# Kernel optimization log

Hardware: AMD Instinct MI355X
Metric: run time of the kernel (lower is better)

Reference implementation:

```python
import jax, jax.numpy as jnp
import numpy as np

B, D, S, E = 32768, 512, 128, 8


def setup_inputs() -> dict:
    key = jax.random.key(0)
    ks = jax.random.split(key, 8)
    x = jax.random.normal(ks[0], (B, D), dtype=jnp.float32)
    y_index = jax.random.randint(ks[1], (B, 1), 0, E, dtype=jnp.int32)
    y_hard = jax.random.uniform(ks[2], (B, E), dtype=jnp.float32)
    z = jax.random.normal(ks[3], (B, 1), dtype=jnp.float32)
    # per-branch 2-layer MLP params, kaiming-ish scaling
    W1 = jax.random.normal(ks[4], (E, D, S), dtype=jnp.float32) / np.sqrt(D)
    b1 = jax.random.normal(ks[5], (E, S), dtype=jnp.float32) * 0.01
    W2 = jax.random.normal(ks[6], (E, S, D), dtype=jnp.float32) / np.sqrt(S)
    b2 = jax.random.normal(ks[7], (E, D), dtype=jnp.float32) * 0.01
    return {"x": x, "y_index": y_index, "y_hard": y_hard, "z": z,
            "W1": W1, "b1": b1, "W2": W2, "b2": b2}


def reference(x, y_index, y_hard, z, W1, b1, W2, b2):
    # out = relu(x); each token b routed to branch y_index[b];
    # branch MLP: relu(out @ W1[e] + b1[e]) @ W2[e] + b2[e], scaled by z, plus residual.
    # y_hard unused (eval path / backward_on_y_hard=False).
    n_branches = W1.shape[0]
    yi = y_index[:, 0]                                   # [B]
    onehot = jax.nn.one_hot(yi, n_branches, dtype=x.dtype)  # [B,E]
    out = jax.nn.relu(x)                                 # [B,D]
    h = jax.nn.relu(jnp.einsum('bd,eds->bes', out, W1) + b1[None])  # [B,E,S]
    h_sel = jnp.einsum('bes,be->bs', h, onehot)          # [B,S] hidden of routed branch
    o = jnp.einsum('bs,esd->bed', h_sel, W2)             # [B,E,D]
    o_sel = jnp.einsum('bed,be->bd', o, onehot) + b2[yi] # [B,D]
    return x + o_sel * z
```

## Files before the change

kernel.cpp:

```cpp
#include <hip/hip_runtime.h>
#include <hip/hip_bf16.h>

#define NB 32768
#define ND 512
#define NS 128
#define NE 8
#define TPE 96

typedef __attribute__((ext_vector_type(8))) short bf16x8;
typedef __attribute__((ext_vector_type(4))) float f32x4;

__device__ __forceinline__ unsigned short f2b(float f) {
  union { __hip_bfloat16 h; unsigned short u; } cv;
  cv.h = __float2bfloat16(f);
  return cv.u;
}

__device__ __forceinline__ bf16x8 relu_cvt8v(float4 a, float4 b) {
  bf16x8 r;
  r[0] = (short)f2b(fmaxf(a.x, 0.f)); r[1] = (short)f2b(fmaxf(a.y, 0.f));
  r[2] = (short)f2b(fmaxf(a.z, 0.f)); r[3] = (short)f2b(fmaxf(a.w, 0.f));
  r[4] = (short)f2b(fmaxf(b.x, 0.f)); r[5] = (short)f2b(fmaxf(b.y, 0.f));
  r[6] = (short)f2b(fmaxf(b.z, 0.f)); r[7] = (short)f2b(fmaxf(b.w, 0.f));
  return r;
}

__device__ __forceinline__ void gload16(const void* gsrc, void* ldst) {
  __builtin_amdgcn_global_load_lds(
      (const __attribute__((address_space(1))) unsigned int*)gsrc,
      (__attribute__((address_space(3))) unsigned int*)ldst, 16, 0, 0);
}

#define BARV6  asm volatile("s_waitcnt vmcnt(6)\n\ts_barrier" ::: "memory")
#define BARV12 asm volatile("s_waitcnt vmcnt(12)\n\ts_barrier" ::: "memory")
#define BARV10 asm volatile("s_waitcnt vmcnt(10)\n\ts_barrier" ::: "memory")
#define BARV0  asm volatile("s_waitcnt vmcnt(0)\n\ts_barrier" ::: "memory")
#define BARL   asm volatile("s_waitcnt lgkmcnt(0)\n\ts_barrier" ::: "memory")
#define BARV2L asm volatile("s_waitcnt vmcnt(2) lgkmcnt(0)\n\ts_barrier" ::: "memory")
#define CFENCE asm volatile("" ::: "memory")

__global__ void zero_counts_k(int* counts) {
  if (threadIdx.x < NE) counts[threadIdx.x] = 0;
}

__global__ void bin_rows_k(const int* __restrict__ yidx, int* __restrict__ counts,
                           int* __restrict__ bucket) {
  __shared__ int lcnt[NE];
  __shared__ int lbase[NE];
  int tid = threadIdx.x;
  if (tid < NE) lcnt[tid] = 0;
  __syncthreads();
  int b = blockIdx.x * blockDim.x + tid;
  int e = yidx[b];
  int pos = atomicAdd(&lcnt[e], 1);
  __syncthreads();
  if (tid < NE) lbase[tid] = atomicAdd(&counts[tid], lcnt[tid]);
  __syncthreads();
  bucket[e * NB + lbase[e] + pos] = b;
}

__global__ void transpose_cvt_k(const float* __restrict__ in,
                                unsigned short* __restrict__ out, int R, int C) {
  __shared__ float lt[32][33];
  int tpm = (R >> 5) * (C >> 5);
  int mat = blockIdx.x / tpm;
  int rem = blockIdx.x % tpm;
  int tcn = C >> 5;
  int tr = rem / tcn, tc = rem % tcn;
  const float* mi = in + (size_t)mat * R * C;
  unsigned short* mo = out + (size_t)mat * R * C;
  int r = threadIdx.x >> 5, c = threadIdx.x & 31;
#pragma unroll
  for (int i = 0; i < 4; ++i) {
    int rr = r + i * 8;
    lt[rr][c] = mi[(size_t)(tr * 32 + rr) * C + tc * 32 + c];
  }
  __syncthreads();
#pragma unroll
  for (int i = 0; i < 4; ++i) {
    int rr = r + i * 8;
    int orow = tc * 32 + rr;
    int d = tr * 32 + c;
    int ocol = (d & ~63) | ((d & 63) ^ ((orow & 7) << 3));
    mo[(size_t)orow * R + ocol] = f2b(lt[c][rr]);
  }
}

#define M1LOADX(DST, c)                                 \
  do {                                                  \
    const float* xp = xrow + (c) * 64;                  \
    DST[0] = *(const float4*)(xp);                      \
    DST[1] = *(const float4*)(xp + 4);                  \
    DST[2] = *(const float4*)(xp + 32);                 \
    DST[3] = *(const float4*)(xp + 36);                 \
  } while (0)

#define M1STAGE(c)                                                        \
  do {                                                                    \
    gload16(g0 + (c) * 128, (char*)wt[(c) % 3] + p0 * 16);                \
    gload16(g1 + (c) * 128, (char*)wt[(c) % 3] + p1 * 16);                \
  } while (0)

#define M1_ITER(c, CUR)                                                        \
  do {                                                                         \
    if ((c) <= 5) { M1STAGE((c) + 2); }                                        \
    bf16x8 a0 = relu_cvt8v(CUR[0], CUR[1]);                                    \
    bf16x8 a1 = relu_cvt8v(CUR[2], CUR[3]);                                    \
    if ((c) <= 5) { M1LOADX(CUR, (c) + 2); }                                   \
    const unsigned short* wb = wt[(c) % 3];                                    \
    __builtin_amdgcn_s_setprio(1);                                             \
    _Pragma("unroll") for (int nt = 0; nt < 4; ++nt) {                         \
      int n = nh * 64 + nt * 16 + l15;                                         \
      int sw = (n & 7) << 3;                                                   \
      bf16x8 b0 = *(const bf16x8*)&wb[n * 64 + ((l4 * 8) ^ sw)];               \
      bf16x8 b1v = *(const bf16x8*)&wb[n * 64 + ((32 + l4 * 8) ^ sw)];         \
      acc[nt] = __builtin_amdgcn_mfma_f32_16x16x32_bf16(a0, b0, acc[nt], 0, 0, 0);  \
      acc[nt] = __builtin_amdgcn_mfma_f32_16x16x32_bf16(a1, b1v, acc[nt], 0, 0, 0); \
    }                                                                          \
    __builtin_amdgcn_s_setprio(0);                                             \
    if ((c) <= 5) { BARV6; } else if ((c) == 6) { BARV0; }                     \
  } while (0)

#define M2STAGE(c)                                                           \
  do {                                                                       \
    gload16(w2e + (c) * 16384 + p0 * 16, (char*)wt[(c) % 3] + p0 * 16);      \
    gload16(w2e + (c) * 16384 + p1 * 16, (char*)wt[(c) % 3] + p1 * 16);      \
  } while (0)

#define M2_ITER(c)                                                            \
  do {                                                                        \
    if ((c) <= 5) { M2STAGE((c) + 2); }                                       \
    float xe0[4], xe1[4];                                                     \
    int d0 = (c) * 64 + nh * 32 + l15;                                        \
    int d1 = d0 + 16;                                                         \
    _Pragma("unroll") for (int r = 0; r < 4; ++r) {                           \
      xe0[r] = x[(size_t)orow[r] * ND + d0];                                  \
      xe1[r] = x[(size_t)orow[r] * ND + d1];                                  \
    }                                                                         \
    float bias0 = b2[e * ND + d0];                                            \
    float bias1 = b2[e * ND + d1];                                            \
    const unsigned short* wb = wt[(c) % 3];                                   \
    f32x4 acc0 = (f32x4){0.f, 0.f, 0.f, 0.f};                                 \
    f32x4 acc1 = (f32x4){0.f, 0.f, 0.f, 0.f};                                 \
    __builtin_amdgcn_s_setprio(1);                                            \
    _Pragma("unroll") for (int kk = 0; kk < 4; ++kk) {                        \
      int dl0 = nh * 32 + l15;                                                \
      int sw0 = (dl0 & 7) << 3;                                               \
      bf16x8 bv0 = *(const bf16x8*)&wb[dl0 * 128 + ((kk * 32 + l4 * 8) ^ sw0)]; \
      acc0 = __builtin_amdgcn_mfma_f32_16x16x32_bf16(ha[kk], bv0, acc0, 0, 0, 0); \
      int dl1 = nh * 32 + 16 + l15;                                           \
      int sw1 = (dl1 & 7) << 3;                                               \
      bf16x8 bv1 = *(const bf16x8*)&wb[dl1 * 128 + ((kk * 32 + l4 * 8) ^ sw1)]; \
      acc1 = __builtin_amdgcn_mfma_f32_16x16x32_bf16(ha[kk], bv1, acc1, 0, 0, 0); \
    }                                                                         \
    __builtin_amdgcn_s_setprio(0);                                            \
    _Pragma("unroll") for (int r = 0; r < 4; ++r) {                           \
      float r0 = xe0[r] + (acc0[r] + bias0) * zr[r];                          \
      float r1 = xe1[r] + (acc1[r] + bias1) * zr[r];                          \
      float* p0s = valid[r] ? (out + (size_t)orow[r] * ND + d0) : (osink + tid); \
      float* p1s = valid[r] ? (out + (size_t)orow[r] * ND + d1) : (osink + tid); \
      *p0s = r0;                                                              \
      *p1s = r1;                                                              \
    }                                                                         \
    if ((c) <= 5) { BARV12; } else if ((c) == 6) { BARV10; }                  \
  } while (0)

__launch_bounds__(512, 6)
__global__ void moe_f(const float* __restrict__ x, const float* __restrict__ z,
                      const float* __restrict__ b1, const float* __restrict__ b2,
                      const unsigned short* __restrict__ w1sw,
                      const unsigned short* __restrict__ w2sw,
                      const int* __restrict__ counts, const int* __restrict__ bucket,
                      float* __restrict__ out, float* __restrict__ osink) {
  __shared__ unsigned short wt[3][8192];
  char* htb = (char*)wt[2];
  int e = blockIdx.x & 7;
  int t = blockIdx.x >> 3;
  int cnt = counts[e];
  if (t * 64 >= cnt) return;
  int tid = threadIdx.x, w = tid >> 6, lane = tid & 63;
  int l15 = lane & 15, l4 = lane >> 4;
  int rg = w >> 1, nh = w & 1;

  int ra = t * 64 + rg * 16 + l15;
  int ras = (ra < cnt) ? ra : (cnt - 1);
  int rid = bucket[e * NB + ras];
  const float* xrow = x + (size_t)rid * ND + l4 * 8;

  const char* w1e = (const char*)w1sw + (size_t)e * NS * ND * 2;
  const char* w2e = (const char*)w2sw + (size_t)e * ND * NS * 2;
  int p0 = tid, p1 = tid + 512;
  const char* g0 = w1e + (p0 >> 3) * 1024 + (p0 & 7) * 16;
  const char* g1 = w1e + (p1 >> 3) * 1024 + (p1 & 7) * 16;

  float4 xA[4], xB[4];
  M1LOADX(xA, 0);
  M1STAGE(0);
  CFENCE;
  M1LOADX(xB, 1);
  M1STAGE(1);
  BARV6;

  f32x4 acc[4];
#pragma unroll
  for (int i = 0; i < 4; ++i) acc[i] = (f32x4){0.f, 0.f, 0.f, 0.f};

  M1_ITER(0, xA); M1_ITER(1, xB); M1_ITER(2, xA); M1_ITER(3, xB);
  M1_ITER(4, xA); M1_ITER(5, xB); M1_ITER(6, xA); M1_ITER(7, xB);

#pragma unroll
  for (int nt = 0; nt < 4; ++nt) {
    int col = nh * 64 + nt * 16 + l15;
    float bias = b1[e * NS + col];
#pragma unroll
    for (int r = 0; r < 4; ++r) {
      int row = rg * 16 + l4 * 4 + r;
      int off = (row * 256 + col * 2) ^ ((row & 7) << 4);
      *(unsigned short*)(htb + off) = f2b(fmaxf(acc[nt][r] + bias, 0.f));
    }
  }

  int orow[4];
  bool valid[4];
  float zr[4];
#pragma unroll
  for (int r = 0; r < 4; ++r) {
    int pos = t * 64 + rg * 16 + l4 * 4 + r;
    valid[r] = (pos < cnt);
    int ps = valid[r] ? pos : (cnt - 1);
    orow[r] = bucket[e * NB + ps];
    zr[r] = z[orow[r]];
  }

  M2STAGE(0);
  BARL;
  M2STAGE(1);

  bf16x8 ha[4];
#pragma unroll
  for (int kk = 0; kk < 4; ++kk) {
    int row = rg * 16 + l15;
    int off = (row * 256 + (kk * 32 + l4 * 8) * 2) ^ ((row & 7) << 4);
    ha[kk] = *(const bf16x8*)(htb + off);
  }
  BARV2L;

  M2_ITER(0); M2_ITER(1); M2_ITER(2); M2_ITER(3);
  M2_ITER(4); M2_ITER(5); M2_ITER(6); M2_ITER(7);
}

extern "C" void kernel_launch(void* const* d_in, const int* in_sizes, int n_in,
                              void* d_out, int out_size, void* d_ws, size_t ws_size,
                              hipStream_t stream) {
  const float* x = (const float*)d_in[0];
  const int* yidx = (const int*)d_in[1];
  const float* z = (const float*)d_in[3];
  const float* W1 = (const float*)d_in[4];
  const float* b1 = (const float*)d_in[5];
  const float* W2 = (const float*)d_in[6];
  const float* b2 = (const float*)d_in[7];
  float* out = (float*)d_out;

  char* ws = (char*)d_ws;
  int* counts = (int*)ws;
  int* bucket = (int*)(ws + 256);
  size_t off = 256 + (size_t)NE * NB * 4;
  unsigned short* w1sw = (unsigned short*)(ws + off);
  off += (size_t)NE * NS * ND * 2;
  unsigned short* w2sw = (unsigned short*)(ws + off);
  off += (size_t)NE * ND * NS * 2;
  float* osink = (float*)(ws + off);

  zero_counts_k<<<1, 64, 0, stream>>>(counts);
  bin_rows_k<<<NB / 1024, 1024, 0, stream>>>(yidx, counts, bucket);
  transpose_cvt_k<<<NE * (ND / 32) * (NS / 32), 256, 0, stream>>>(W1, w1sw, ND, NS);
  transpose_cvt_k<<<NE * (NS / 32) * (ND / 32), 256, 0, stream>>>(W2, w2sw, NS, ND);
  moe_f<<<NE * TPE, 512, 0, stream>>>(x, z, b1, b2, w1sw, w2sw, counts, bucket,
                                      out, osink);
}
```

Baseline: 67.39 us.

## Defer second-GEMM epilogue until after all W2 chunks, keeping accumulators in registers

Output accumulators for all eight W2 column chunks are now held in registers, and the residual/bias/scale epilogue with its x reads and out stores runs once after the MFMA loop. The barriers inside the loop then only wait on the weight-tile loads, not on interleaved x loads and stores. Invalid rows are skipped with a branch instead of being written to a sink buffer. The cost is 64 more accumulator registers per thread, so launch bounds drop from 6 to 4 waves' worth, reducing occupancy, and the epilogue memory traffic no longer overlaps with compute.

After: 73.31 us. 8.8% more time.

```diff
diff --git a/kernel.cpp b/kernel.cpp
--- a/kernel.cpp
+++ b/kernel.cpp
@@ -32,8 +32,7 @@
 }
 
 #define BARV6  asm volatile("s_waitcnt vmcnt(6)\n\ts_barrier" ::: "memory")
-#define BARV12 asm volatile("s_waitcnt vmcnt(12)\n\ts_barrier" ::: "memory")
-#define BARV10 asm volatile("s_waitcnt vmcnt(10)\n\ts_barrier" ::: "memory")
+#define BARV2  asm volatile("s_waitcnt vmcnt(2)\n\ts_barrier" ::: "memory")
 #define BARV0  asm volatile("s_waitcnt vmcnt(0)\n\ts_barrier" ::: "memory")
 #define BARL   asm volatile("s_waitcnt lgkmcnt(0)\n\ts_barrier" ::: "memory")
 #define BARV2L asm volatile("s_waitcnt vmcnt(2) lgkmcnt(0)\n\ts_barrier" ::: "memory")
@@ -130,48 +129,31 @@
 #define M2_ITER(c)                                                            \
   do {                                                                        \
     if ((c) <= 5) { M2STAGE((c) + 2); }                                       \
-    float xe0[4], xe1[4];                                                     \
-    int d0 = (c) * 64 + nh * 32 + l15;                                        \
-    int d1 = d0 + 16;                                                         \
-    _Pragma("unroll") for (int r = 0; r < 4; ++r) {                           \
-      xe0[r] = x[(size_t)orow[r] * ND + d0];                                  \
-      xe1[r] = x[(size_t)orow[r] * ND + d1];                                  \
-    }                                                                         \
-    float bias0 = b2[e * ND + d0];                                            \
-    float bias1 = b2[e * ND + d1];                                            \
     const unsigned short* wb = wt[(c) % 3];                                   \
-    f32x4 acc0 = (f32x4){0.f, 0.f, 0.f, 0.f};                                 \
-    f32x4 acc1 = (f32x4){0.f, 0.f, 0.f, 0.f};                                 \
     __builtin_amdgcn_s_setprio(1);                                            \
     _Pragma("unroll") for (int kk = 0; kk < 4; ++kk) {                        \
       int dl0 = nh * 32 + l15;                                                \
       int sw0 = (dl0 & 7) << 3;                                               \
       bf16x8 bv0 = *(const bf16x8*)&wb[dl0 * 128 + ((kk * 32 + l4 * 8) ^ sw0)]; \
-      acc0 = __builtin_amdgcn_mfma_f32_16x16x32_bf16(ha[kk], bv0, acc0, 0, 0, 0); \
+      acc2[c][0] = __builtin_amdgcn_mfma_f32_16x16x32_bf16(ha[kk], bv0,       \
+                                                           acc2[c][0], 0, 0, 0); \
       int dl1 = nh * 32 + 16 + l15;                                           \
       int sw1 = (dl1 & 7) << 3;                                               \
       bf16x8 bv1 = *(const bf16x8*)&wb[dl1 * 128 + ((kk * 32 + l4 * 8) ^ sw1)]; \
-      acc1 = __builtin_amdgcn_mfma_f32_16x16x32_bf16(ha[kk], bv1, acc1, 0, 0, 0); \
+      acc2[c][1] = __builtin_amdgcn_mfma_f32_16x16x32_bf16(ha[kk], bv1,       \
+                                                           acc2[c][1], 0, 0, 0); \
     }                                                                         \
     __builtin_amdgcn_s_setprio(0);                                            \
-    _Pragma("unroll") for (int r = 0; r < 4; ++r) {                           \
-      float r0 = xe0[r] + (acc0[r] + bias0) * zr[r];                          \
-      float r1 = xe1[r] + (acc1[r] + bias1) * zr[r];                          \
-      float* p0s = valid[r] ? (out + (size_t)orow[r] * ND + d0) : (osink + tid); \
-      float* p1s = valid[r] ? (out + (size_t)orow[r] * ND + d1) : (osink + tid); \
-      *p0s = r0;                                                              \
-      *p1s = r1;                                                              \
-    }                                                                         \
-    if ((c) <= 5) { BARV12; } else if ((c) == 6) { BARV10; }                  \
-  } while (0)
-
-__launch_bounds__(512, 6)
+    if ((c) <= 5) { BARV2; } else if ((c) == 6) { BARV0; }                    \
+  } while (0)
+
+__launch_bounds__(512, 4)
 __global__ void moe_f(const float* __restrict__ x, const float* __restrict__ z,
                       const float* __restrict__ b1, const float* __restrict__ b2,
                       const unsigned short* __restrict__ w1sw,
                       const unsigned short* __restrict__ w2sw,
                       const int* __restrict__ counts, const int* __restrict__ bucket,
-                      float* __restrict__ out, float* __restrict__ osink) {
+                      float* __restrict__ out) {
   __shared__ unsigned short wt[3][8192];
   char* htb = (char*)wt[2];
   int e = blockIdx.x & 7;
@@ -245,8 +227,32 @@
   }
   BARV2L;
 
+  f32x4 acc2[8][2];
+#pragma unroll
+  for (int i = 0; i < 8; ++i) {
+    acc2[i][0] = (f32x4){0.f, 0.f, 0.f, 0.f};
+    acc2[i][1] = (f32x4){0.f, 0.f, 0.f, 0.f};
+  }
+
   M2_ITER(0); M2_ITER(1); M2_ITER(2); M2_ITER(3);
   M2_ITER(4); M2_ITER(5); M2_ITER(6); M2_ITER(7);
+
+#pragma unroll
+  for (int c = 0; c < 8; ++c) {
+    int d0 = c * 64 + nh * 32 + l15;
+    int d1 = d0 + 16;
+    float bias0 = b2[e * ND + d0];
+    float bias1 = b2[e * ND + d1];
+#pragma unroll
+    for (int r = 0; r < 4; ++r) {
+      if (valid[r]) {
+        size_t o0 = (size_t)orow[r] * ND + d0;
+        size_t o1 = (size_t)orow[r] * ND + d1;
+        out[o0] = x[o0] + (acc2[c][0][r] + bias0) * zr[r];
+        out[o1] = x[o1] + (acc2[c][1][r] + bias1) * zr[r];
+      }
+    }
+  }
 }
 
 extern "C" void kernel_launch(void* const* d_in, const int* in_sizes, int n_in,
@@ -268,13 +274,10 @@
   unsigned short* w1sw = (unsigned short*)(ws + off);
   off += (size_t)NE * NS * ND * 2;
   unsigned short* w2sw = (unsigned short*)(ws + off);
-  off += (size_t)NE * ND * NS * 2;
-  float* osink = (float*)(ws + off);
 
   zero_counts_k<<<1, 64, 0, stream>>>(counts);
   bin_rows_k<<<NB / 1024, 1024, 0, stream>>>(yidx, counts, bucket);
   transpose_cvt_k<<<NE * (ND / 32) * (NS / 32), 256, 0, stream>>>(W1, w1sw, ND, NS);
   transpose_cvt_k<<<NE * (NS / 32) * (ND / 32), 256, 0, stream>>>(W2, w2sw, NS, ND);
-  moe_f<<<NE * TPE, 512, 0, stream>>>(x, z, b1, b2, w1sw, w2sw, counts, bucket,
-                                      out, osink);
-}
+  moe_f<<<NE * TPE, 512, 0, stream>>>(x, z, b1, b2, w1sw, w2sw, counts, bucket, out);
+}
```
